# Performance work log

Measured on AMD Instinct MI355X. Metric: run time of the kernel, lower is better.

## Reference

```python
import jax, jax.numpy as jnp
import numpy as np

N_STEPS = 128
B = 32768
H = 64
T0, T1 = 0.0, 1.0
L = 1.0
DT = (T1 - T0) / N_STEPS

# ---- synthesized Equation methods (shapes match the torch forward) ----
def U_fn(x):            return jnp.sum(x * x, axis=-1, keepdims=True)            # [.., B, 1]
def D_fn(n):            return 0.5 + 0.1 * jnp.abs(n)                            # [B, 1] > 0
def alpha_fn(n):        return 0.5 * (n + 1.0)
def beta_fn(n):         return 0.4 * jnp.abs(n) + 0.1
def sigma0_fn(x):       # [B,3,3]
    return 0.5 * jnp.eye(3, dtype=x.dtype) + 0.1 * x[..., :, None] * x[..., None, :]
def T_inv_fn(x):        # [B,3,3]
    nrm = 1.0 + jnp.sum(x * x, axis=-1)[..., None, None]
    return jnp.eye(3, dtype=x.dtype) - x[..., :, None] * x[..., None, :] / nrm
def f_fn(t, n, x, p, y, z):  # y complex [B,1], z complex [B,3]
    return p * y + 0.1 * (1.0 + t) * jnp.sum(z, axis=-1, keepdims=True)
def g_fn(n, x):
    return jnp.sum(x, axis=-1, keepdims=True).astype(jnp.complex64)

def mlp_c(W1, b1, W2, b2, inp):
    """MLP with complex output via paired real/imag heads."""
    h = jnp.tanh(inp @ W1 + b1)
    o = h @ W2 + b2
    d = o.shape[-1] // 2
    return (o[..., :d] + 1j * o[..., d:]).astype(jnp.complex64)

def feat(n, x, p):
    return jnp.concatenate([n, x, p], axis=-1)  # [B, 5]


def setup_inputs() -> dict:
    key = jax.random.key(0)
    ks = jax.random.split(key, 16)
    # polar sample -> 3D start point on the sphere (tran_2to3)
    theta = jax.random.uniform(ks[0], (B, 1)) * jnp.pi
    phi = jax.random.uniform(ks[1], (B, 1)) * 2.0 * jnp.pi
    x0 = jnp.concatenate([jnp.sin(theta) * jnp.cos(phi),
                          jnp.sin(theta) * jnp.sin(phi),
                          jnp.cos(theta)], axis=-1)                       # [B,3]
    # Brownian increments and paths (get_position)
    delta_B = jnp.sqrt(DT) * jax.random.normal(ks[2], (N_STEPS, B, 3), jnp.float32)
    process_X = jnp.concatenate([x0[None], x0[None] + jnp.cumsum(delta_B, 0)], 0)  # [N+1,B,3]
    # birth-death jump counting process
    dN = (jax.random.randint(ks[3], (N_STEPS, B, 1), 0, 3) - 1).astype(jnp.float32)
    n0 = jnp.full((1, B, 1), 10.0, jnp.float32)
    process_N = jnp.concatenate([n0, n0 + jnp.cumsum(dN, 0)], 0)           # [N+1,B,1]
    discrete_p = jax.random.uniform(ks[4], (N_STEPS + 1, B, 1), jnp.float32)
    discrete_t = jnp.linspace(T0, T1, N_STEPS + 1, dtype=jnp.float32)

    def w(k, shape, fan_in):
        return jax.random.normal(k, shape, jnp.float32) / np.sqrt(fan_in)
    inp = dict(process_N=process_N, process_X=process_X, discrete_p=discrete_p,
               discrete_t=discrete_t, delta_B=delta_B,
               Wr1=w(ks[5], (5, H), 5), br1=jnp.zeros((H,)),
               Wr2=w(ks[6], (H, 2), H), br2=jnp.zeros((2,)),
               Wg1=w(ks[7], (N_STEPS, 5, H), 5), bg1=jnp.zeros((N_STEPS, H)),
               Wg2=w(ks[8], (N_STEPS, H, 6), H), bg2=jnp.zeros((N_STEPS, 6)),
               Wj1=w(ks[9], (N_STEPS, 5, H), 5), bj1=jnp.zeros((N_STEPS, H)),
               Wj2=w(ks[10], (N_STEPS, H, 2), H), bj2=jnp.zeros((N_STEPS, 2)))
    return inp


def bsde_forward(process_N, process_X, discrete_p, discrete_t, delta_B,
                 Wr1, br1, Wr2, br2, Wg1, bg1, Wg2, bg2, Wj1, bj1, Wj2, bj2):
    # functional bookkeeping: exp(-cumsum(roll(1j*p*U(x),1) with [0]=0) * dt)
    functional = 1j * discrete_p * U_fn(process_X)                         # [N+1,B,1] c64
    functional = jnp.concatenate([jnp.zeros_like(functional[:1]), functional[:-1]], 0)
    exp_functional = jnp.exp(-jnp.cumsum(functional, axis=0) * DT)         # [N+1,B,1] c64

    u0 = mlp_c(Wr1, br1, Wr2, br2, feat(process_N[0], process_X[0], discrete_p[0]))  # [B,1]
    delta_N_all = jnp.round(process_N[1:] - process_N[:-1])                # [N,B,1]

    xs = (process_N[:-1], process_X[:-1], discrete_p[:-1], discrete_t[:-1],
          delta_B, exp_functional[:-1], delta_N_all,
          Wg1, bg1, Wg2, bg2, Wj1, bj1, Wj2, bj2)

    def step(u, xi):
        (n, x, p, t, dB, ef, dNi, wg1, bg1_, wg2, bg2_, wj1, bj1_, wj2, bj2_) = xi
        ft = feat(n, x, p)
        grad_u = mlp_c(wg1, bg1_, wg2, bg2_, ft)                           # [B,3] c64
        S = sigma0_fn(x)                                                   # [B,3,3]
        Ti = T_inv_fn(x)                                                   # [B,3,3]
        k = jnp.sqrt(2.0 * D_fn(n)) / L                                    # [B,1]
        kg = k * grad_u                                                    # [B,3] c64
        M = jnp.einsum('bij,bkj->bik', Ti, S).astype(jnp.complex64)        # T_inv @ sigma^T
        grad_bmm = jnp.einsum('bi,bij,bj->b', kg, M,
                              dB.astype(jnp.complex64))[:, None]           # [B,1] c64
        ui  = mlp_c(wj1, bj1_, wj2, bj2_, ft)
        uip = mlp_c(wj1, bj1_, wj2, bj2_, feat(n + 1.0, x, p))
        uim = mlp_c(wj1, bj1_, wj2, bj2_, feat(n - 1.0, x, p))
        dup, dum = uip - ui, uim - ui
        fv = f_fn(t, n, x, p, u / ef, grad_u)
        delt = grad_bmm - (alpha_fn(n) * dup + beta_fn(n) * dum) * DT - fv * DT
        delt = jnp.where(dNi > 0, dup, jnp.where(dNi < 0, dum, delt))
        return u + ef * delt, None

    u, _ = jax.lax.scan(step, u0, xs)
    g = exp_functional[-1] * g_fn(process_N[-1], process_X[-1])
    return u, g


def reference(process_N, process_X, discrete_p, discrete_t, delta_B,
              Wr1, br1, Wr2, br2, Wg1, bg1, Wg2, bg2, Wj1, bj1, Wj2, bj2):
    return bsde_forward(process_N, process_X, discrete_p, discrete_t, delta_B,
                        Wr1, br1, Wr2, br2, Wg1, bg1, Wg2, bg2, Wj1, bj1, Wj2, bj2)
```

## Files before the change

### kernel.cpp

```cpp
#include <hip/hip_runtime.h>
#include <math.h>

#define NSTEPS 128
#define BATCH  32768
#define HID    64

constexpr float DTf = 1.0f / 128.0f;
constexpr float TWO_LOG2E = 2.88539008177792681f;

typedef float v2f __attribute__((ext_vector_type(2)));

__device__ __forceinline__ v2f v2ld(const float* p) { return *(const v2f*)p; }

struct CD { float c, dre, dim; };

__device__ __forceinline__ float fast_tanh(float x) {
    float e = __builtin_amdgcn_exp2f(x * TWO_LOG2E);
    return 1.0f - 2.0f * __builtin_amdgcn_rcpf(e + 1.0f);
}
__device__ __forceinline__ v2f fast_tanh2(v2f z) {
    v2f zs = z * TWO_LOG2E;
    v2f e;
    e.x = __builtin_amdgcn_exp2f(zs.x);
    e.y = __builtin_amdgcn_exp2f(zs.y);
    v2f e1 = e + 1.0f;
    v2f r;
    r.x = __builtin_amdgcn_rcpf(e1.x);
    r.y = __builtin_amdgcn_rcpf(e1.y);
    return 1.0f - 2.0f * r;
}

__device__ __forceinline__ void grad_mlp(
    float n, float x0, float x1, float x2, float p,
    const float* __restrict__ w1, const float* __restrict__ b1,
    const float* __restrict__ w2, const float* __restrict__ b2,
    float& og0, float& og1, float& og2, float& og3, float& og4, float& og5)
{
    v2f og01 = { b2[0], b2[1] };
    v2f og23 = { b2[2], b2[3] };
    v2f og45 = { b2[4], b2[5] };
#pragma unroll 4
    for (int j = 0; j < HID; j += 2) {
        v2f z = n  * v2ld(w1 + j)
              + x0 * v2ld(w1 + HID   + j)
              + x1 * v2ld(w1 + 2*HID + j)
              + x2 * v2ld(w1 + 3*HID + j)
              + p  * v2ld(w1 + 4*HID + j)
              + v2ld(b1 + j);
        v2f h = fast_tanh2(z);
        const float* wj = w2 + j*6;
        og01 += h.x * v2ld(wj)     + h.y * v2ld(wj + 6);
        og23 += h.x * v2ld(wj + 2) + h.y * v2ld(wj + 8);
        og45 += h.x * v2ld(wj + 4) + h.y * v2ld(wj + 10);
    }
    og0 = og01.x; og1 = og01.y; og2 = og23.x;
    og3 = og23.y; og4 = og45.x; og5 = og45.y;
}

template<bool USE_TD>
__device__ __forceinline__ void jump_mlp(
    float n, float x0, float x1, float x2, float p,
    const float* __restrict__ v1, const float* __restrict__ c1,
    const float* __restrict__ vw2, const float* __restrict__ Td,
    float& dup0, float& dup1, float& dum0, float& dum1)
{
    v2f dup01 = { 0.f, 0.f };
    v2f dum01 = { 0.f, 0.f };
#pragma unroll 4
    for (int j = 0; j < HID; j += 2) {
        v2f d  = v2ld(v1 + j);
        v2f zb = n  * d
               + x0 * v2ld(v1 + HID   + j)
               + x1 * v2ld(v1 + 2*HID + j)
               + x2 * v2ld(v1 + 3*HID + j)
               + p  * v2ld(v1 + 4*HID + j)
               + v2ld(c1 + j);
        v2f T  = fast_tanh2(zb);
        v2f Tv;
        if (USE_TD) Tv = v2ld(Td + j);
        else { Tv.x = fast_tanh(d.x); Tv.y = fast_tanh(d.y); }
        v2f a    = T * Tv;
        v2f oma2 = 1.0f - a*a;
        v2f r;
        r.x = __builtin_amdgcn_rcpf(oma2.x);
        r.y = __builtin_amdgcn_rcpf(oma2.y);
        v2f ep = (T + Tv) * (1.0f - a) * r - T;
        v2f em = (T - Tv) * (1.0f + a) * r - T;
        v2f wv0 = v2ld(vw2 + 2*j);
        v2f wv1 = v2ld(vw2 + 2*j + 2);
        dup01 += ep.x * wv0 + ep.y * wv1;
        dum01 += em.x * wv0 + em.y * wv1;
    }
    dup0 = dup01.x; dup1 = dup01.y;
    dum0 = dum01.x; dum1 = dum01.y;
}

template<bool USE_TD>
__device__ __forceinline__ CD step_core(
    float n, float x0, float x1, float x2, float p, float t,
    float db0, float db1, float db2, float dN, float phi,
    const float* __restrict__ w1, const float* __restrict__ b1,
    const float* __restrict__ w2, const float* __restrict__ b2,
    const float* __restrict__ v1, const float* __restrict__ c1,
    const float* __restrict__ vw2, const float* __restrict__ Td)
{
    float og0, og1, og2, og3, og4, og5;
    grad_mlp(n,x0,x1,x2,p, w1,b1,w2,b2, og0,og1,og2,og3,og4,og5);
    float dup0, dup1, dum0, dum1;
    jump_mlp<USE_TD>(n,x0,x1,x2,p, v1,c1,vw2,Td, dup0,dup1,dum0,dum1);

    float r2    = fmaf(x0,x0, fmaf(x1,x1, x2*x2));
    float gamma = 0.1f - (0.5f + 0.1f*r2) * __builtin_amdgcn_rcpf(1.0f + r2);
    float xdb   = fmaf(x0,db0, fmaf(x1,db1, x2*db2));
    float kc    = sqrtf(fmaf(0.2f, fabsf(n), 1.0f));
    float gdb_r = fmaf(og0,db0, fmaf(og1,db1, og2*db2));
    float gdb_i = fmaf(og3,db0, fmaf(og4,db1, og5*db2));
    float gx_r  = fmaf(og0,x0,  fmaf(og1,x1,  og2*x2));
    float gx_i  = fmaf(og3,x0,  fmaf(og4,x1,  og5*x2));
    float gb_r  = kc * fmaf(gamma*xdb, gx_r, 0.5f*gdb_r);
    float gb_i  = kc * fmaf(gamma*xdb, gx_i, 0.5f*gdb_i);

    float alpha = 0.5f*(n + 1.0f);
    float beta  = fmaf(0.4f, fabsf(n), 0.1f);
    float cf    = 0.1f*(1.0f + t)*DTf;
    float d0r = gb_r - (alpha*dup0 + beta*dum0)*DTf - cf*(og0+og1+og2);
    float d0i = gb_i - (alpha*dup1 + beta*dum1)*DTf - cf*(og3+og4+og5);

    float c, sr, si;
    if (dN > 0.5f)       { c = 1.0f;          sr = dup0; si = dup1; }
    else if (dN < -0.5f) { c = 1.0f;          sr = dum0; si = dum1; }
    else                 { c = 1.0f - p*DTf;  sr = d0r;  si = d0i;  }

    float sp, cp;
    __sincosf(phi, &sp, &cp);
    CD o;
    o.c   = c;
    o.dre = fmaf(cp, sr,  sp*si);
    o.dim = fmaf(cp, si, -sp*sr);
    return o;
}

__device__ __forceinline__ void mlp_u0(
    float n, float x0, float x1, float x2, float p,
    const float* __restrict__ w1, const float* __restrict__ b1,
    const float* __restrict__ w2, const float* __restrict__ b2,
    float& ur, float& ui)
{
    v2f o01 = { b2[0], b2[1] };
#pragma unroll 4
    for (int j = 0; j < HID; j += 2) {
        v2f z = n  * v2ld(w1 + j)
              + x0 * v2ld(w1 + HID   + j)
              + x1 * v2ld(w1 + 2*HID + j)
              + x2 * v2ld(w1 + 3*HID + j)
              + p  * v2ld(w1 + 4*HID + j)
              + v2ld(b1 + j);
        v2f h = fast_tanh2(z);
        o01 += h.x * v2ld(w2 + 2*j) + h.y * v2ld(w2 + 2*j + 2);
    }
    ur = o01.x; ui = o01.y;
}

__global__ void __launch_bounds__(256) k_phi(
    const float* __restrict__ X, const float* __restrict__ P,
    float* __restrict__ phi, float* __restrict__ phiF)
{
    int b = blockIdx.x*256 + threadIdx.x;
    double s = 0.0;
    for (int k = 0; k < NSTEPS; k++) {
        size_t idx = (size_t)k*BATCH + b;
        phi[idx] = (float)(DTf * s);
        float p = P[idx];
        const float* xp = X + idx*3;
        float x0 = xp[0], x1 = xp[1], x2 = xp[2];
        s += (double)p * (double)(x0*x0 + x1*x1 + x2*x2);
    }
    phiF[b] = (float)(DTf * s);
}

__global__ void __launch_bounds__(256) k_step(
    const float* __restrict__ N,  const float* __restrict__ X,
    const float* __restrict__ P,  const float* __restrict__ Tarr,
    const float* __restrict__ dB,
    const float* __restrict__ Wg1, const float* __restrict__ bg1,
    const float* __restrict__ Wg2, const float* __restrict__ bg2,
    const float* __restrict__ Wj1, const float* __restrict__ bj1,
    const float* __restrict__ Wj2, const float* __restrict__ bj2,
    const float* __restrict__ phiA, float* __restrict__ cA, float2* __restrict__ dA)
{
    int k = blockIdx.y;
    const float* w1 = Wg1 + k*5*HID;
    const float* b1 = bg1 + k*HID;
    const float* w2 = Wg2 + k*HID*6;
    const float* b2 = bg2 + k*6;
    const float* v1 = Wj1 + k*5*HID;
    const float* c1 = bj1 + k*HID;
    const float* vw2 = Wj2 + k*HID*2;
    float t = Tarr[k];

    __shared__ float Td[HID];
    __shared__ float sdat[256][13];
    __shared__ int   sorig[256];
    __shared__ int   cnt[2];
    if (threadIdx.x < HID) Td[threadIdx.x] = fast_tanh(v1[threadIdx.x]);
    if (threadIdx.x == 0) { cnt[0] = 0; cnt[1] = 0; }
    __syncthreads();

    int tid = threadIdx.x;
    int b = blockIdx.x*256 + tid;
    size_t idx = (size_t)k*BATCH + b;
    {
        float n  = N[idx], p = P[idx];
        const float* xp  = X  + idx*3;
        const float* dbp = dB + idx*3;
        float dN = N[idx + BATCH] - n;
        bool full = (dN == 0.0f);
        int pos = full ? atomicAdd(&cnt[0], 1) : 255 - atomicAdd(&cnt[1], 1);
        sorig[pos]  = b;
        float* sd = sdat[pos];
        sd[0]=n;      sd[1]=p;      sd[2]=xp[0]; sd[3]=xp[1]; sd[4]=xp[2];
        sd[5]=dbp[0]; sd[6]=dbp[1]; sd[7]=dbp[2];
        sd[8]=phiA[idx]; sd[9]=dN;
    }
    __syncthreads();

    const float* md = sdat[tid];
    float n   = md[0], p   = md[1];
    float x0  = md[2], x1  = md[3], x2 = md[4];
    float db0 = md[5], db1 = md[6], db2 = md[7];
    float phi = md[8], dN  = md[9];
    int   ob  = sorig[tid];
    bool  g   = (dN == 0.0f);

    float dup0, dup1, dum0, dum1;
    jump_mlp<true>(n,x0,x1,x2,p, v1,c1,vw2,Td, dup0,dup1,dum0,dum1);

    float og0=0.f, og1=0.f, og2=0.f, og3=0.f, og4=0.f, og5=0.f;
    if (__ballot(g) != 0ull) {
        grad_mlp(n,x0,x1,x2,p, w1,b1,w2,b2, og0,og1,og2,og3,og4,og5);
    }

    float r2    = fmaf(x0,x0, fmaf(x1,x1, x2*x2));
    float gamma = 0.1f - (0.5f + 0.1f*r2) * __builtin_amdgcn_rcpf(1.0f + r2);
    float xdb   = fmaf(x0,db0, fmaf(x1,db1, x2*db2));
    float kc    = sqrtf(fmaf(0.2f, fabsf(n), 1.0f));
    float gdb_r = fmaf(og0,db0, fmaf(og1,db1, og2*db2));
    float gdb_i = fmaf(og3,db0, fmaf(og4,db1, og5*db2));
    float gx_r  = fmaf(og0,x0,  fmaf(og1,x1,  og2*x2));
    float gx_i  = fmaf(og3,x0,  fmaf(og4,x1,  og5*x2));
    float gb_r  = kc * fmaf(gamma*xdb, gx_r, 0.5f*gdb_r);
    float gb_i  = kc * fmaf(gamma*xdb, gx_i, 0.5f*gdb_i);

    float alpha = 0.5f*(n + 1.0f);
    float beta  = fmaf(0.4f, fabsf(n), 0.1f);
    float cf    = 0.1f*(1.0f + t)*DTf;
    float d0r = gb_r - (alpha*dup0 + beta*dum0)*DTf - cf*(og0+og1+og2);
    float d0i = gb_i - (alpha*dup1 + beta*dum1)*DTf - cf*(og3+og4+og5);

    float c, sr, si;
    if (dN > 0.5f)       { c = 1.0f;          sr = dup0; si = dup1; }
    else if (dN < -0.5f) { c = 1.0f;          sr = dum0; si = dum1; }
    else                 { c = 1.0f - p*DTf;  sr = d0r;  si = d0i;  }

    float sp, cp;
    __sincosf(phi, &sp, &cp);

    size_t oidx = (size_t)k*BATCH + ob;
    cA[oidx] = c;
    dA[oidx] = make_float2(fmaf(cp, sr,  sp*si), fmaf(cp, si, -sp*sr));
}

__global__ void __launch_bounds__(256) k_combine(
    const float* __restrict__ N, const float* __restrict__ X, const float* __restrict__ P,
    const float* __restrict__ Wr1, const float* __restrict__ br1,
    const float* __restrict__ Wr2, const float* __restrict__ br2,
    const float* __restrict__ cA, const float2* __restrict__ dA,
    const float* __restrict__ phiF, float* __restrict__ out, int full)
{
    int b = blockIdx.x*256 + threadIdx.x;
    const float* xp = X + (size_t)b*3;
    float ur, ui;
    mlp_u0(N[b], xp[0], xp[1], xp[2], P[b], Wr1, br1, Wr2, br2, ur, ui);
#pragma unroll 8
    for (int k = 0; k < NSTEPS; k++) {
        size_t idx = (size_t)k*BATCH + b;
        float  c = cA[idx];
        float2 d = dA[idx];
        ur = fmaf(c, ur, d.x);
        ui = fmaf(c, ui, d.y);
    }
    float phi = phiF[b];
    const float* xf = X + ((size_t)NSTEPS*BATCH + b)*3;
    float s = xf[0] + xf[1] + xf[2];
    float sp, cp;
    __sincosf(phi, &sp, &cp);
    float gre =  s*cp;
    float gim = -s*sp;
    if (full) {
        out[b]           = ur;
        out[BATCH + b]   = ui;
        out[2*BATCH + b] = gre;
        out[3*BATCH + b] = gim;
    } else {
        out[b]         = ur;
        out[BATCH + b] = gre;
    }
}

__global__ void __launch_bounds__(256) k_fused(
    const float* __restrict__ N,  const float* __restrict__ X,
    const float* __restrict__ P,  const float* __restrict__ Tarr,
    const float* __restrict__ dB,
    const float* __restrict__ Wr1, const float* __restrict__ br1,
    const float* __restrict__ Wr2, const float* __restrict__ br2,
    const float* __restrict__ Wg1, const float* __restrict__ bg1,
    const float* __restrict__ Wg2, const float* __restrict__ bg2,
    const float* __restrict__ Wj1, const float* __restrict__ bj1,
    const float* __restrict__ Wj2, const float* __restrict__ bj2,
    float* __restrict__ out, int full)
{
    int b = blockIdx.x*256 + threadIdx.x;
    float ur, ui;
    {
        const float* xp = X + (size_t)b*3;
        mlp_u0(N[b], xp[0], xp[1], xp[2], P[b], Wr1, br1, Wr2, br2, ur, ui);
    }
    double s = 0.0;
    for (int k = 0; k < NSTEPS; k++) {
        size_t idx = (size_t)k*BATCH + b;
        float n = N[idx], p = P[idx], t = Tarr[k];
        const float* xp  = X  + idx*3;
        const float* dbp = dB + idx*3;
        float dN  = N[idx + BATCH] - n;
        float phi = (float)(DTf * s);
        CD cd = step_core<false>(n, xp[0], xp[1], xp[2], p, t,
                                 dbp[0], dbp[1], dbp[2], dN, phi,
                                 Wg1 + k*5*HID, bg1 + k*HID,
                                 Wg2 + k*HID*6, bg2 + k*6,
                                 Wj1 + k*5*HID, bj1 + k*HID,
                                 Wj2 + k*HID*2, nullptr);
        ur = fmaf(cd.c, ur, cd.dre);
        ui = fmaf(cd.c, ui, cd.dim);
        float x0 = xp[0], x1 = xp[1], x2 = xp[2];
        s += (double)p * (double)(x0*x0 + x1*x1 + x2*x2);
    }
    float phi = (float)(DTf * s);
    const float* xf = X + ((size_t)NSTEPS*BATCH + b)*3;
    float sm = xf[0] + xf[1] + xf[2];
    float sp, cp;
    __sincosf(phi, &sp, &cp);
    float gre =  sm*cp;
    float gim = -sm*sp;
    if (full) {
        out[b]           = ur;
        out[BATCH + b]   = ui;
        out[2*BATCH + b] = gre;
        out[3*BATCH + b] = gim;
    } else {
        out[b]         = ur;
        out[BATCH + b] = gre;
    }
}

extern "C" void kernel_launch(void* const* d_in, const int* in_sizes, int n_in,
                              void* d_out, int out_size, void* d_ws, size_t ws_size,
                              hipStream_t stream)
{
    const float* N    = (const float*)d_in[0];
    const float* X    = (const float*)d_in[1];
    const float* P    = (const float*)d_in[2];
    const float* Tarr = (const float*)d_in[3];
    const float* dB   = (const float*)d_in[4];
    const float* Wr1  = (const float*)d_in[5];
    const float* br1  = (const float*)d_in[6];
    const float* Wr2  = (const float*)d_in[7];
    const float* br2  = (const float*)d_in[8];
    const float* Wg1  = (const float*)d_in[9];
    const float* bg1  = (const float*)d_in[10];
    const float* Wg2  = (const float*)d_in[11];
    const float* bg2  = (const float*)d_in[12];
    const float* Wj1  = (const float*)d_in[13];
    const float* bj1  = (const float*)d_in[14];
    const float* Wj2  = (const float*)d_in[15];
    const float* bj2  = (const float*)d_in[16];
    float* out = (float*)d_out;

    const int full = (out_size >= 4*BATCH) ? 1 : 0;

    const size_t phi_elems = (size_t)NSTEPS*BATCH;
    const size_t need = (phi_elems + BATCH + phi_elems)*sizeof(float)
                      + phi_elems*sizeof(float2);

    if (ws_size >= need) {
        float*  phiA = (float*)d_ws;
        float*  phiF = phiA + phi_elems;
        float*  cA   = phiF + BATCH;
        float2* dA   = (float2*)(cA + phi_elems);

        k_phi<<<dim3(BATCH/256), dim3(256), 0, stream>>>(X, P, phiA, phiF);
        k_step<<<dim3(BATCH/256, NSTEPS), dim3(256), 0, stream>>>(
            N, X, P, Tarr, dB, Wg1, bg1, Wg2, bg2, Wj1, bj1, Wj2, bj2,
            phiA, cA, dA);
        k_combine<<<dim3(BATCH/256), dim3(256), 0, stream>>>(
            N, X, P, Wr1, br1, Wr2, br2, cA, dA, phiF, out, full);
    } else {
        k_fused<<<dim3(BATCH/256), dim3(256), 0, stream>>>(
            N, X, P, Tarr, dB, Wr1, br1, Wr2, br2,
            Wg1, bg1, Wg2, bg2, Wj1, bj1, Wj2, bj2, out, full);
    }
}
```

Measured before the change: 239.8 us.

## Compute only the needed jump branch for wavefronts made entirely of jump samples

Warps whose samples all jump (dN != 0) now run a single-sided jump MLP that evaluates only the up or down difference chosen by the sign of dN, and skip the gradient MLP and diffusion terms. Warps that contain any non-jump sample still run both MLPs. The block size grows to 512 so the in-block compaction of jump and non-jump samples produces more uniform wavefronts, at some cost in occupancy and shared memory. The jump-difference arithmetic is also refactored into multiply-add friendly form.

```diff
diff --git a/kernel.cpp b/kernel.cpp
--- a/kernel.cpp
+++ b/kernel.cpp
@@ -4,6 +4,7 @@
 #define NSTEPS 128
 #define BATCH  32768
 #define HID    64
+#define BLK    512
 
 constexpr float DTf = 1.0f / 128.0f;
 constexpr float TWO_LOG2E = 2.88539008177792681f;
@@ -84,8 +85,12 @@
         v2f r;
         r.x = __builtin_amdgcn_rcpf(oma2.x);
         r.y = __builtin_amdgcn_rcpf(oma2.y);
-        v2f ep = (T + Tv) * (1.0f - a) * r - T;
-        v2f em = (T - Tv) * (1.0f + a) * r - T;
+        v2f s1 = (T + Tv) * r;
+        v2f u1 = s1 - T;
+        v2f ep = u1 - s1*a;
+        v2f s2 = (T - Tv) * r;
+        v2f u2 = s2 - T;
+        v2f em = u2 + s2*a;
         v2f wv0 = v2ld(vw2 + 2*j);
         v2f wv1 = v2ld(vw2 + 2*j + 2);
         dup01 += ep.x * wv0 + ep.y * wv1;
@@ -93,6 +98,37 @@
     }
     dup0 = dup01.x; dup1 = dup01.y;
     dum0 = dum01.x; dum1 = dum01.y;
+}
+
+__device__ __forceinline__ void jump_mlp_1s(
+    float n, float x0, float x1, float x2, float p, float sgn,
+    const float* __restrict__ v1, const float* __restrict__ c1,
+    const float* __restrict__ vw2, const float* __restrict__ Td,
+    float& e0, float& e1)
+{
+    v2f acc = { 0.f, 0.f };
+#pragma unroll 4
+    for (int j = 0; j < HID; j += 2) {
+        v2f d  = v2ld(v1 + j);
+        v2f zb = n  * d
+               + x0 * v2ld(v1 + HID   + j)
+               + x1 * v2ld(v1 + 2*HID + j)
+               + x2 * v2ld(v1 + 3*HID + j)
+               + p  * v2ld(v1 + 4*HID + j)
+               + v2ld(c1 + j);
+        v2f T   = fast_tanh2(zb);
+        v2f Tsv = sgn * v2ld(Td + j);
+        v2f as  = T * Tsv;
+        v2f oma = 1.0f - as*as;
+        v2f r;
+        r.x = __builtin_amdgcn_rcpf(oma.x);
+        r.y = __builtin_amdgcn_rcpf(oma.y);
+        v2f s1 = (T + Tsv) * r;
+        v2f u1 = s1 - T;
+        v2f e  = u1 - s1*as;
+        acc += e.x * v2ld(vw2 + 2*j) + e.y * v2ld(vw2 + 2*j + 2);
+    }
+    e0 = acc.x; e1 = acc.y;
 }
 
 template<bool USE_TD>
@@ -178,7 +214,7 @@
     phiF[b] = (float)(DTf * s);
 }
 
-__global__ void __launch_bounds__(256) k_step(
+__global__ void __launch_bounds__(BLK) k_step(
     const float* __restrict__ N,  const float* __restrict__ X,
     const float* __restrict__ P,  const float* __restrict__ Tarr,
     const float* __restrict__ dB,
@@ -199,15 +235,15 @@
     float t = Tarr[k];
 
     __shared__ float Td[HID];
-    __shared__ float sdat[256][13];
-    __shared__ int   sorig[256];
+    __shared__ float sdat[BLK][13];
+    __shared__ int   sorig[BLK];
     __shared__ int   cnt[2];
     if (threadIdx.x < HID) Td[threadIdx.x] = fast_tanh(v1[threadIdx.x]);
     if (threadIdx.x == 0) { cnt[0] = 0; cnt[1] = 0; }
     __syncthreads();
 
     int tid = threadIdx.x;
-    int b = blockIdx.x*256 + tid;
+    int b = blockIdx.x*BLK + tid;
     size_t idx = (size_t)k*BATCH + b;
     {
         float n  = N[idx], p = P[idx];
@@ -215,7 +251,7 @@
         const float* dbp = dB + idx*3;
         float dN = N[idx + BATCH] - n;
         bool full = (dN == 0.0f);
-        int pos = full ? atomicAdd(&cnt[0], 1) : 255 - atomicAdd(&cnt[1], 1);
+        int pos = full ? atomicAdd(&cnt[0], 1) : (BLK-1) - atomicAdd(&cnt[1], 1);
         sorig[pos]  = b;
         float* sd = sdat[pos];
         sd[0]=n;      sd[1]=p;      sd[2]=xp[0]; sd[3]=xp[1]; sd[4]=xp[2];
@@ -232,39 +268,40 @@
     int   ob  = sorig[tid];
     bool  g   = (dN == 0.0f);
 
-    float dup0, dup1, dum0, dum1;
-    jump_mlp<true>(n,x0,x1,x2,p, v1,c1,vw2,Td, dup0,dup1,dum0,dum1);
-
-    float og0=0.f, og1=0.f, og2=0.f, og3=0.f, og4=0.f, og5=0.f;
+    float c, sr, si;
     if (__ballot(g) != 0ull) {
+        float dup0, dup1, dum0, dum1;
+        jump_mlp<true>(n,x0,x1,x2,p, v1,c1,vw2,Td, dup0,dup1,dum0,dum1);
+        float og0, og1, og2, og3, og4, og5;
         grad_mlp(n,x0,x1,x2,p, w1,b1,w2,b2, og0,og1,og2,og3,og4,og5);
-    }
-
-    float r2    = fmaf(x0,x0, fmaf(x1,x1, x2*x2));
-    float gamma = 0.1f - (0.5f + 0.1f*r2) * __builtin_amdgcn_rcpf(1.0f + r2);
-    float xdb   = fmaf(x0,db0, fmaf(x1,db1, x2*db2));
-    float kc    = sqrtf(fmaf(0.2f, fabsf(n), 1.0f));
-    float gdb_r = fmaf(og0,db0, fmaf(og1,db1, og2*db2));
-    float gdb_i = fmaf(og3,db0, fmaf(og4,db1, og5*db2));
-    float gx_r  = fmaf(og0,x0,  fmaf(og1,x1,  og2*x2));
-    float gx_i  = fmaf(og3,x0,  fmaf(og4,x1,  og5*x2));
-    float gb_r  = kc * fmaf(gamma*xdb, gx_r, 0.5f*gdb_r);
-    float gb_i  = kc * fmaf(gamma*xdb, gx_i, 0.5f*gdb_i);
-
-    float alpha = 0.5f*(n + 1.0f);
-    float beta  = fmaf(0.4f, fabsf(n), 0.1f);
-    float cf    = 0.1f*(1.0f + t)*DTf;
-    float d0r = gb_r - (alpha*dup0 + beta*dum0)*DTf - cf*(og0+og1+og2);
-    float d0i = gb_i - (alpha*dup1 + beta*dum1)*DTf - cf*(og3+og4+og5);
-
-    float c, sr, si;
-    if (dN > 0.5f)       { c = 1.0f;          sr = dup0; si = dup1; }
-    else if (dN < -0.5f) { c = 1.0f;          sr = dum0; si = dum1; }
-    else                 { c = 1.0f - p*DTf;  sr = d0r;  si = d0i;  }
+
+        float r2    = fmaf(x0,x0, fmaf(x1,x1, x2*x2));
+        float gamma = 0.1f - (0.5f + 0.1f*r2) * __builtin_amdgcn_rcpf(1.0f + r2);
+        float xdb   = fmaf(x0,db0, fmaf(x1,db1, x2*db2));
+        float kc    = sqrtf(fmaf(0.2f, fabsf(n), 1.0f));
+        float gdb_r = fmaf(og0,db0, fmaf(og1,db1, og2*db2));
+        float gdb_i = fmaf(og3,db0, fmaf(og4,db1, og5*db2));
+        float gx_r  = fmaf(og0,x0,  fmaf(og1,x1,  og2*x2));
+        float gx_i  = fmaf(og3,x0,  fmaf(og4,x1,  og5*x2));
+        float gb_r  = kc * fmaf(gamma*xdb, gx_r, 0.5f*gdb_r);
+        float gb_i  = kc * fmaf(gamma*xdb, gx_i, 0.5f*gdb_i);
+
+        float alpha = 0.5f*(n + 1.0f);
+        float beta  = fmaf(0.4f, fabsf(n), 0.1f);
+        float cf    = 0.1f*(1.0f + t)*DTf;
+        float d0r = gb_r - (alpha*dup0 + beta*dum0)*DTf - cf*(og0+og1+og2);
+        float d0i = gb_i - (alpha*dup1 + beta*dum1)*DTf - cf*(og3+og4+og5);
+
+        if (dN > 0.5f)       { c = 1.0f;          sr = dup0; si = dup1; }
+        else if (dN < -0.5f) { c = 1.0f;          sr = dum0; si = dum1; }
+        else                 { c = 1.0f - p*DTf;  sr = d0r;  si = d0i;  }
+    } else {
+        jump_mlp_1s(n,x0,x1,x2,p, dN, v1,c1,vw2,Td, sr, si);
+        c = 1.0f;
+    }
 
     float sp, cp;
     __sincosf(phi, &sp, &cp);
-
     size_t oidx = (size_t)k*BATCH + ob;
     cA[oidx] = c;
     dA[oidx] = make_float2(fmaf(cp, sr,  sp*si), fmaf(cp, si, -sp*sr));
@@ -398,7 +435,7 @@
         float2* dA   = (float2*)(cA + phi_elems);
 
         k_phi<<<dim3(BATCH/256), dim3(256), 0, stream>>>(X, P, phiA, phiF);
-        k_step<<<dim3(BATCH/256, NSTEPS), dim3(256), 0, stream>>>(
+        k_step<<<dim3(BATCH/BLK, NSTEPS), dim3(BLK), 0, stream>>>(
             N, X, P, Tarr, dB, Wg1, bg1, Wg2, bg2, Wj1, bj1, Wj2, bj2,
             phiA, cA, dA);
         k_combine<<<dim3(BATCH/256), dim3(256), 0, stream>>>(
```

Measured after the change: 218.8 us. 1.1x faster.
